# Optimization experiments

Hardware: AMD Instinct MI355X
Metric: run time of the kernel (lower is better)

Reference implementation:

```python
import jax, jax.numpy as jnp
import numpy as np

L = 4      # number of layers (graph nodes)
B = 128    # batch
H = 4096   # neurons per layer


def setup_inputs() -> dict:
    key = jax.random.key(0)
    k1, k2, k3 = jax.random.split(key, 3)
    # per-layer source activations, stacked: [L, B, H]
    states = jax.random.normal(k1, (L, B, H), dtype=jnp.float32)
    # all Connection weight matrices, W[t, s] maps source s -> target t: [L, L, H_out, H_in]
    # scaled by 1/sqrt(H) so summed matmuls stay O(1) (original uses constant w_init)
    W = jax.random.normal(k2, (L, L, H, H), dtype=jnp.float32) * (1.0 / np.sqrt(H))
    # external inputs added into each target's current: [L, B, H]
    ext = jax.random.normal(k3, (L, B, H), dtype=jnp.float32)
    return {"states": states, "W": W, "ext": ext}


def reference(states, W, ext):
    # Synapses/Links: for each target t, sum over sources s of (x_s @ W[t,s].T)
    # (Connection.forward is x @ w.T). Single fused einsum replaces the
    # jit.fork fan-out over L*L small matmuls + Python-level sum.
    currents = jnp.einsum('sbh,tsoh->tbo', states, W) + ext  # [L, B, H]
    # Layer/Neurons: per-node activation function
    return jnp.tanh(currents)
```

## Files before the change

kernel.cpp:

```cpp
#include <hip/hip_runtime.h>
#include <hip/hip_bf16.h>
#include <stdint.h>

#define L_ 4
#define B_ 128
#define H_ 4096
#define BK 64
#define BN 32
#define KSTEPS 256
#define NTHR 256
#define ABYTES (128*BK*2)
#define WBYTES (BN*BK*2)
#define BUFBYTES (ABYTES+WBYTES)

typedef _Float16 f16x8 __attribute__((ext_vector_type(8)));
typedef float    f32x4 __attribute__((ext_vector_type(4)));
typedef float    f4    __attribute__((ext_vector_type(4)));
typedef uint32_t u32x4 __attribute__((ext_vector_type(4)));
typedef uint32_t u32x2 __attribute__((ext_vector_type(2)));

__device__ __forceinline__ uint32_t pack2(float a, float b) {
  const _Float16 ha = (_Float16)a;
  const _Float16 hb = (_Float16)b;
  const uint32_t ua = (uint32_t)__builtin_bit_cast(uint16_t, ha);
  const uint32_t ub = (uint32_t)__builtin_bit_cast(uint16_t, hb);
  return ua | (ub << 16);
}

__global__ void cvt_states_kernel(const float* __restrict__ x,
                                  uint32_t* __restrict__ y, int n4) {
  const int i = blockIdx.x * blockDim.x + threadIdx.x;
  if (i < n4) {
    f4 v = reinterpret_cast<const f4*>(x)[i];
    u32x2 o;
    o.x = pack2(v.x, v.y);
    o.y = pack2(v.z, v.w);
    reinterpret_cast<u32x2*>(y)[i] = o;
  }
}

__device__ __forceinline__ void bar_lgkm0() {
  __builtin_amdgcn_sched_barrier(0);
  asm volatile("s_waitcnt lgkmcnt(0)");
  __builtin_amdgcn_sched_barrier(0);
  __builtin_amdgcn_s_barrier();
  __builtin_amdgcn_sched_barrier(0);
}

template<bool USE_WS>
__global__ __launch_bounds__(NTHR, 2)
void net_gemm_kernel(const float* __restrict__ statesf,
                     const uint16_t* __restrict__ statesh,
                     const float* __restrict__ Wm,
                     const float* __restrict__ ext,
                     float* __restrict__ out)
{
  __shared__ uint8_t lds[2 * BUFBYTES];

  const int tid  = threadIdx.x;
  const int bid  = blockIdx.x;
  const int t    = bid >> 7;
  const int n0   = (bid & 127) * BN;

  const int wv   = tid >> 6;
  const int lane = tid & 63;
  const int lid  = lane & 15;
  const int lh   = lane >> 4;

  const int arow = tid >> 3;
  const int acol = (tid & 7) * 8;
  const uint32_t a_st_off =
      (uint32_t)arow * 128 + (((uint32_t)(tid & 7) * 16) ^ ((uint32_t)(arow & 7) << 4));
  const uint16_t* ah_base = USE_WS ? (statesh + (size_t)arow * H_ + acol) : nullptr;
  const float*    af_base = statesf + (size_t)arow * H_ + acol;

  const int wrow = tid >> 4;
  const int wcol = (tid & 15) * 4;
  const float* w_base = Wm + ((size_t)t * L_ * H_ + (size_t)(n0 + wrow)) * H_ + wcol;
  const uint32_t w_st_off0 =
      (uint32_t)ABYTES + (uint32_t)wrow * 128 + (((uint32_t)(tid & 15) * 8) ^ ((uint32_t)(wrow & 7) << 4));
  const uint32_t w_st_off1 = w_st_off0 + 16 * 128;

  uint32_t a_rd[2][2], b_rd[2][2];
  #pragma unroll
  for (int mf = 0; mf < 2; ++mf)
    #pragma unroll
    for (int kk = 0; kk < 2; ++kk) {
      const int row = wv * 32 + mf * 16 + lid;
      a_rd[mf][kk] = (uint32_t)row * 128 +
                     (((uint32_t)(kk * 64 + lh * 16)) ^ ((uint32_t)(lid & 7) << 4));
    }
  #pragma unroll
  for (int nf = 0; nf < 2; ++nf)
    #pragma unroll
    for (int kk = 0; kk < 2; ++kk) {
      const int row = nf * 16 + lid;
      b_rd[nf][kk] = (uint32_t)ABYTES + (uint32_t)row * 128 +
                     (((uint32_t)(kk * 64 + lh * 16)) ^ ((uint32_t)(lid & 7) << 4));
    }

  f32x4 acc[2][2] = {};

  u32x4 ah0[4], ah1[4];
  f4    af0[4][2], af1[4][2];
  f4    wf0[2], wf1[2];

  auto LOADg = [&](int kidx, u32x4 (&ah)[4], f4 (&af)[4][2], f4 (&wf)[2]) {
    const int s  = kidx >> 6;
    const int h0 = (kidx & 63) << 6;
    if constexpr (USE_WS) {
      const uint16_t* ap = ah_base + (size_t)s * (B_ * H_) + h0;
      #pragma unroll
      for (int j = 0; j < 4; ++j)
        ah[j] = *reinterpret_cast<const u32x4*>(ap + (size_t)j * (32 * H_));
    } else {
      const float* ap = af_base + (size_t)s * (B_ * H_) + h0;
      #pragma unroll
      for (int j = 0; j < 4; ++j) {
        af[j][0] = *reinterpret_cast<const f4*>(ap + (size_t)j * (32 * H_));
        af[j][1] = *reinterpret_cast<const f4*>(ap + (size_t)j * (32 * H_) + 4);
      }
    }
    const float* wp = Wm == nullptr ? nullptr : (w_base + (size_t)s * ((size_t)H_ * H_) + h0);
    wf[0] = __builtin_nontemporal_load(reinterpret_cast<const f4*>(wp));
    wf[1] = __builtin_nontemporal_load(reinterpret_cast<const f4*>(wp + 16 * (size_t)H_));
  };

  auto WRITEg = [&](uint8_t* base, u32x4 (&ah)[4], f4 (&af)[4][2], f4 (&wf)[2]) {
    if constexpr (USE_WS) {
      #pragma unroll
      for (int j = 0; j < 4; ++j)
        *reinterpret_cast<u32x4*>(base + j * 4096 + a_st_off) = ah[j];
    } else {
      #pragma unroll
      for (int j = 0; j < 4; ++j) {
        u32x4 v;
        v.x = pack2(af[j][0].x, af[j][0].y);
        v.y = pack2(af[j][0].z, af[j][0].w);
        v.z = pack2(af[j][1].x, af[j][1].y);
        v.w = pack2(af[j][1].z, af[j][1].w);
        *reinterpret_cast<u32x4*>(base + j * 4096 + a_st_off) = v;
      }
    }
    u32x2 w0, w1;
    w0.x = pack2(wf[0].x, wf[0].y); w0.y = pack2(wf[0].z, wf[0].w);
    w1.x = pack2(wf[1].x, wf[1].y); w1.y = pack2(wf[1].z, wf[1].w);
    *reinterpret_cast<u32x2*>(base + w_st_off0) = w0;
    *reinterpret_cast<u32x2*>(base + w_st_off1) = w1;
  };

  auto COMPUTE = [&](const uint8_t* base) {
    f16x8 av[2][2], bv[2][2];
    #pragma unroll
    for (int mf = 0; mf < 2; ++mf)
      #pragma unroll
      for (int kk = 0; kk < 2; ++kk)
        av[mf][kk] = *reinterpret_cast<const f16x8*>(base + a_rd[mf][kk]);
    #pragma unroll
    for (int nf = 0; nf < 2; ++nf)
      #pragma unroll
      for (int kk = 0; kk < 2; ++kk)
        bv[nf][kk] = *reinterpret_cast<const f16x8*>(base + b_rd[nf][kk]);
    #pragma unroll
    for (int kk = 0; kk < 2; ++kk)
      #pragma unroll
      for (int mf = 0; mf < 2; ++mf)
        #pragma unroll
        for (int nf = 0; nf < 2; ++nf)
          acc[mf][nf] = __builtin_amdgcn_mfma_f32_16x16x32_f16(
              av[mf][kk], bv[nf][kk], acc[mf][nf], 0, 0, 0);
  };

  uint8_t* buf0 = lds;
  uint8_t* buf1 = lds + BUFBYTES;

  LOADg(0, ah0, af0, wf0);
  LOADg(1, ah1, af1, wf1);
  WRITEg(buf0, ah0, af0, wf0);
  bar_lgkm0();

  #pragma unroll 1
  for (int k = 0; k < KSTEPS; k += 2) {
    if (k + 2 < KSTEPS) LOADg(k + 2, ah0, af0, wf0);
    COMPUTE(buf0);
    WRITEg(buf1, ah1, af1, wf1);
    bar_lgkm0();

    if (k + 3 < KSTEPS) LOADg(k + 3, ah1, af1, wf1);
    COMPUTE(buf1);
    if (k + 2 < KSTEPS) {
      WRITEg(buf0, ah0, af0, wf0);
      bar_lgkm0();
    }
  }

  #pragma unroll
  for (int mf = 0; mf < 2; ++mf)
    #pragma unroll
    for (int nf = 0; nf < 2; ++nf)
      #pragma unroll
      for (int j = 0; j < 4; ++j) {
        const int brow = wv * 32 + mf * 16 + lh * 4 + j;
        const int ocol = n0 + nf * 16 + lid;
        const size_t idx = ((size_t)(t * B_ + brow)) * H_ + ocol;
        out[idx] = tanhf(acc[mf][nf][j] + ext[idx]);
      }
}

extern "C" void kernel_launch(void* const* d_in, const int* in_sizes, int n_in,
                              void* d_out, int out_size, void* d_ws, size_t ws_size,
                              hipStream_t stream) {
  const float* states = (const float*)d_in[0];
  const float* W      = (const float*)d_in[1];
  const float* ext    = (const float*)d_in[2];
  float* out          = (float*)d_out;

  const size_t nstates = (size_t)L_ * B_ * H_;
  if (ws_size >= nstates * sizeof(uint16_t)) {
    const int n4 = (int)(nstates / 4);
    cvt_states_kernel<<<(n4 + 255) / 256, 256, 0, stream>>>(states, (uint32_t*)d_ws, n4);
    net_gemm_kernel<true><<<512, NTHR, 0, stream>>>(
        states, (const uint16_t*)d_ws, W, ext, out);
  } else {
    net_gemm_kernel<false><<<512, NTHR, 0, stream>>>(
        states, nullptr, W, ext, out);
  }
}
```

Measured before the change: 250.8 us.

## Load A fragments directly from global into registers and double K tile

Activation (A) fragments are no longer staged through LDS. Each wave now loads its MFMA operands straight from global memory (fp16 workspace or fp32 converted in registers) into registers in the MFMA layout. Only the W tile goes through LDS, and the K tile grows from 64 to 128, which halves the iteration and barrier count. This cuts LDS traffic and footprint, at the cost of more register pressure and less coalesced, strided global reads for A, which mostly come from L2.

```diff
diff --git a/kernel.cpp b/kernel.cpp
--- a/kernel.cpp
+++ b/kernel.cpp
@@ -5,13 +5,11 @@
 #define L_ 4
 #define B_ 128
 #define H_ 4096
-#define BK 64
+#define BK 128
 #define BN 32
-#define KSTEPS 256
+#define KIT 128
 #define NTHR 256
-#define ABYTES (128*BK*2)
 #define WBYTES (BN*BK*2)
-#define BUFBYTES (ABYTES+WBYTES)
 
 typedef _Float16 f16x8 __attribute__((ext_vector_type(8)));
 typedef float    f32x4 __attribute__((ext_vector_type(4)));
@@ -55,7 +53,7 @@
                      const float* __restrict__ ext,
                      float* __restrict__ out)
 {
-  __shared__ uint8_t lds[2 * BUFBYTES];
+  __shared__ uint8_t lds[2 * WBYTES];
 
   const int tid  = threadIdx.x;
   const int bid  = blockIdx.x;
@@ -67,129 +65,115 @@
   const int lid  = lane & 15;
   const int lh   = lane >> 4;
 
-  const int arow = tid >> 3;
-  const int acol = (tid & 7) * 8;
-  const uint32_t a_st_off =
-      (uint32_t)arow * 128 + (((uint32_t)(tid & 7) * 16) ^ ((uint32_t)(arow & 7) << 4));
-  const uint16_t* ah_base = USE_WS ? (statesh + (size_t)arow * H_ + acol) : nullptr;
-  const float*    af_base = statesf + (size_t)arow * H_ + acol;
-
-  const int wrow = tid >> 4;
-  const int wcol = (tid & 15) * 4;
-  const float* w_base = Wm + ((size_t)t * L_ * H_ + (size_t)(n0 + wrow)) * H_ + wcol;
-  const uint32_t w_st_off0 =
-      (uint32_t)ABYTES + (uint32_t)wrow * 128 + (((uint32_t)(tid & 15) * 8) ^ ((uint32_t)(wrow & 7) << 4));
-  const uint32_t w_st_off1 = w_st_off0 + 16 * 128;
-
-  uint32_t a_rd[2][2], b_rd[2][2];
-  #pragma unroll
-  for (int mf = 0; mf < 2; ++mf)
-    #pragma unroll
-    for (int kk = 0; kk < 2; ++kk) {
-      const int row = wv * 32 + mf * 16 + lid;
-      a_rd[mf][kk] = (uint32_t)row * 128 +
-                     (((uint32_t)(kk * 64 + lh * 16)) ^ ((uint32_t)(lid & 7) << 4));
-    }
+  const uint16_t* ah_base = USE_WS ? (statesh + (size_t)(wv * 32 + lid) * H_ + lh * 8) : nullptr;
+  const float*    af_base = statesf + (size_t)(wv * 32 + lid) * H_ + lh * 8;
+
+  const int wrow = tid >> 3;
+  const int wc16 = (tid & 7) * 16;
+  const float* w_base = Wm + ((size_t)(t * L_) * H_ + (size_t)(n0 + wrow)) * H_ + wc16;
+  const uint32_t cb = (uint32_t)(tid & 7) * 32;
+  const uint32_t w_st0 = (uint32_t)wrow * 256 + (cb ^ (((uint32_t)wrow & 7) << 4));
+  const uint32_t w_st1 = (uint32_t)wrow * 256 + ((cb + 16) ^ (((uint32_t)wrow & 7) << 4));
+
+  uint32_t b_rd[2][4];
   #pragma unroll
   for (int nf = 0; nf < 2; ++nf)
     #pragma unroll
-    for (int kk = 0; kk < 2; ++kk) {
-      const int row = nf * 16 + lid;
-      b_rd[nf][kk] = (uint32_t)ABYTES + (uint32_t)row * 128 +
-                     (((uint32_t)(kk * 64 + lh * 16)) ^ ((uint32_t)(lid & 7) << 4));
+    for (int kk = 0; kk < 4; ++kk) {
+      const uint32_t row = (uint32_t)(nf * 16 + lid);
+      b_rd[nf][kk] = row * 256 +
+                     (((uint32_t)(kk * 64 + lh * 16)) ^ (((uint32_t)lid & 7) << 4));
     }
 
   f32x4 acc[2][2] = {};
 
-  u32x4 ah0[4], ah1[4];
-  f4    af0[4][2], af1[4][2];
-  f4    wf0[2], wf1[2];
-
-  auto LOADg = [&](int kidx, u32x4 (&ah)[4], f4 (&af)[4][2], f4 (&wf)[2]) {
-    const int s  = kidx >> 6;
-    const int h0 = (kidx & 63) << 6;
+  f16x8 aA[2][4], aB[2][4];
+  f4    wfA[4], wfB[4];
+
+  auto LOADA = [&](int kidx, f16x8 (&ar)[2][4]) {
+    const int s  = kidx >> 5;
+    const int h0 = (kidx & 31) << 7;
     if constexpr (USE_WS) {
-      const uint16_t* ap = ah_base + (size_t)s * (B_ * H_) + h0;
-      #pragma unroll
-      for (int j = 0; j < 4; ++j)
-        ah[j] = *reinterpret_cast<const u32x4*>(ap + (size_t)j * (32 * H_));
+      const uint16_t* p = ah_base + (size_t)s * (B_ * H_) + h0;
+      #pragma unroll
+      for (int mf = 0; mf < 2; ++mf)
+        #pragma unroll
+        for (int kk = 0; kk < 4; ++kk)
+          ar[mf][kk] = *reinterpret_cast<const f16x8*>(p + mf * (16 * H_) + kk * 32);
     } else {
-      const float* ap = af_base + (size_t)s * (B_ * H_) + h0;
-      #pragma unroll
-      for (int j = 0; j < 4; ++j) {
-        af[j][0] = *reinterpret_cast<const f4*>(ap + (size_t)j * (32 * H_));
-        af[j][1] = *reinterpret_cast<const f4*>(ap + (size_t)j * (32 * H_) + 4);
-      }
+      const float* p = af_base + (size_t)s * (B_ * H_) + h0;
+      #pragma unroll
+      for (int mf = 0; mf < 2; ++mf)
+        #pragma unroll
+        for (int kk = 0; kk < 4; ++kk) {
+          f4 lo = *reinterpret_cast<const f4*>(p + mf * (16 * H_) + kk * 32);
+          f4 hi = *reinterpret_cast<const f4*>(p + mf * (16 * H_) + kk * 32 + 4);
+          u32x4 v;
+          v.x = pack2(lo.x, lo.y); v.y = pack2(lo.z, lo.w);
+          v.z = pack2(hi.x, hi.y); v.w = pack2(hi.z, hi.w);
+          ar[mf][kk] = __builtin_bit_cast(f16x8, v);
+        }
     }
-    const float* wp = Wm == nullptr ? nullptr : (w_base + (size_t)s * ((size_t)H_ * H_) + h0);
-    wf[0] = __builtin_nontemporal_load(reinterpret_cast<const f4*>(wp));
-    wf[1] = __builtin_nontemporal_load(reinterpret_cast<const f4*>(wp + 16 * (size_t)H_));
-  };
-
-  auto WRITEg = [&](uint8_t* base, u32x4 (&ah)[4], f4 (&af)[4][2], f4 (&wf)[2]) {
-    if constexpr (USE_WS) {
-      #pragma unroll
-      for (int j = 0; j < 4; ++j)
-        *reinterpret_cast<u32x4*>(base + j * 4096 + a_st_off) = ah[j];
-    } else {
-      #pragma unroll
-      for (int j = 0; j < 4; ++j) {
-        u32x4 v;
-        v.x = pack2(af[j][0].x, af[j][0].y);
-        v.y = pack2(af[j][0].z, af[j][0].w);
-        v.z = pack2(af[j][1].x, af[j][1].y);
-        v.w = pack2(af[j][1].z, af[j][1].w);
-        *reinterpret_cast<u32x4*>(base + j * 4096 + a_st_off) = v;
-      }
-    }
-    u32x2 w0, w1;
-    w0.x = pack2(wf[0].x, wf[0].y); w0.y = pack2(wf[0].z, wf[0].w);
-    w1.x = pack2(wf[1].x, wf[1].y); w1.y = pack2(wf[1].z, wf[1].w);
-    *reinterpret_cast<u32x2*>(base + w_st_off0) = w0;
-    *reinterpret_cast<u32x2*>(base + w_st_off1) = w1;
-  };
-
-  auto COMPUTE = [&](const uint8_t* base) {
-    f16x8 av[2][2], bv[2][2];
-    #pragma unroll
-    for (int mf = 0; mf < 2; ++mf)
-      #pragma unroll
-      for (int kk = 0; kk < 2; ++kk)
-        av[mf][kk] = *reinterpret_cast<const f16x8*>(base + a_rd[mf][kk]);
+  };
+
+  auto LOADW = [&](int kidx, f4 (&wf)[4]) {
+    const int s  = kidx >> 5;
+    const int h0 = (kidx & 31) << 7;
+    const float* wp = w_base + (size_t)s * ((size_t)H_ * H_) + h0;
+    #pragma unroll
+    for (int j = 0; j < 4; ++j)
+      wf[j] = __builtin_nontemporal_load(reinterpret_cast<const f4*>(wp + j * 4));
+  };
+
+  auto WRITEW = [&](uint8_t* base, f4 (&wf)[4]) {
+    u32x4 v0, v1;
+    v0.x = pack2(wf[0].x, wf[0].y); v0.y = pack2(wf[0].z, wf[0].w);
+    v0.z = pack2(wf[1].x, wf[1].y); v0.w = pack2(wf[1].z, wf[1].w);
+    v1.x = pack2(wf[2].x, wf[2].y); v1.y = pack2(wf[2].z, wf[2].w);
+    v1.z = pack2(wf[3].x, wf[3].y); v1.w = pack2(wf[3].z, wf[3].w);
+    *reinterpret_cast<u32x4*>(base + w_st0) = v0;
+    *reinterpret_cast<u32x4*>(base + w_st1) = v1;
+  };
+
+  auto COMPUTE = [&](const uint8_t* base, f16x8 (&ar)[2][4]) {
+    f16x8 bv[2][4];
     #pragma unroll
     for (int nf = 0; nf < 2; ++nf)
       #pragma unroll
-      for (int kk = 0; kk < 2; ++kk)
+      for (int kk = 0; kk < 4; ++kk)
         bv[nf][kk] = *reinterpret_cast<const f16x8*>(base + b_rd[nf][kk]);
     #pragma unroll
-    for (int kk = 0; kk < 2; ++kk)
+    for (int kk = 0; kk < 4; ++kk)
       #pragma unroll
       for (int mf = 0; mf < 2; ++mf)
         #pragma unroll
         for (int nf = 0; nf < 2; ++nf)
           acc[mf][nf] = __builtin_amdgcn_mfma_f32_16x16x32_f16(
-              av[mf][kk], bv[nf][kk], acc[mf][nf], 0, 0, 0);
+              ar[mf][kk], bv[nf][kk], acc[mf][nf], 0, 0, 0);
   };
 
   uint8_t* buf0 = lds;
-  uint8_t* buf1 = lds + BUFBYTES;
-
-  LOADg(0, ah0, af0, wf0);
-  LOADg(1, ah1, af1, wf1);
-  WRITEg(buf0, ah0, af0, wf0);
+  uint8_t* buf1 = lds + WBYTES;
+
+  LOADW(0, wfA);
+  LOADW(1, wfB);
+  LOADA(0, aA);
+  WRITEW(buf0, wfA);
   bar_lgkm0();
 
   #pragma unroll 1
-  for (int k = 0; k < KSTEPS; k += 2) {
-    if (k + 2 < KSTEPS) LOADg(k + 2, ah0, af0, wf0);
-    COMPUTE(buf0);
-    WRITEg(buf1, ah1, af1, wf1);
+  for (int k = 0; k < KIT; k += 2) {
+    if (k + 2 < KIT) LOADW(k + 2, wfA);
+    LOADA(k + 1, aB);
+    COMPUTE(buf0, aA);
+    WRITEW(buf1, wfB);
     bar_lgkm0();
 
-    if (k + 3 < KSTEPS) LOADg(k + 3, ah1, af1, wf1);
-    COMPUTE(buf1);
-    if (k + 2 < KSTEPS) {
-      WRITEg(buf0, ah0, af0, wf0);
+    if (k + 3 < KIT) LOADW(k + 3, wfB);
+    if (k + 2 < KIT) LOADA(k + 2, aA);
+    COMPUTE(buf1, aB);
+    if (k + 2 < KIT) {
+      WRITEW(buf0, wfA);
       bar_lgkm0();
     }
   }
```

Measured after the change: 430.3 us. 1.72x slower.

## Load activations via direct global-to-LDS copies with triple-buffered pipeline

Applied to the files above, without the earlier changes.

The fp16 activation tile is now copied straight from global memory into LDS with global_load_lds, so it no longer passes through registers. The main loop moves to three LDS buffers, unrolled six ways. Barriers wait on a partial vmcnt so up to two stages of loads can be in flight while MFMAs run. This aims to hide memory latency in the streaming-W GEMM and cut register pressure, at the cost of extra LDS and fragile manual waitcnt bookkeeping; the fp32 fallback path is split into its own kernel.

```diff
diff --git a/kernel.cpp b/kernel.cpp
--- a/kernel.cpp
+++ b/kernel.cpp
@@ -7,11 +7,11 @@
 #define H_ 4096
 #define BK 64
 #define BN 32
-#define KSTEPS 256
+#define KIT 256
 #define NTHR 256
 #define ABYTES (128*BK*2)
 #define WBYTES (BN*BK*2)
-#define BUFBYTES (ABYTES+WBYTES)
+#define BUFB   (ABYTES+WBYTES)
 
 typedef _Float16 f16x8 __attribute__((ext_vector_type(8)));
 typedef float    f32x4 __attribute__((ext_vector_type(4)));
@@ -39,23 +39,27 @@
   }
 }
 
-__device__ __forceinline__ void bar_lgkm0() {
-  __builtin_amdgcn_sched_barrier(0);
-  asm volatile("s_waitcnt lgkmcnt(0)");
-  __builtin_amdgcn_sched_barrier(0);
-  __builtin_amdgcn_s_barrier();
-  __builtin_amdgcn_sched_barrier(0);
-}
-
-template<bool USE_WS>
+__device__ __forceinline__ void gld_lds16(const void* g, void* l) {
+  __builtin_amdgcn_global_load_lds(
+      (const __attribute__((address_space(1))) void*)g,
+      (__attribute__((address_space(3))) void*)l, 16, 0, 0);
+}
+
+#define BAR_VM(N_) do {                                          \
+    __builtin_amdgcn_sched_barrier(0);                           \
+    asm volatile("s_waitcnt vmcnt(" #N_ ") lgkmcnt(0)" ::: "memory"); \
+    __builtin_amdgcn_sched_barrier(0);                           \
+    __builtin_amdgcn_s_barrier();                                \
+    __builtin_amdgcn_sched_barrier(0);                           \
+  } while (0)
+
 __global__ __launch_bounds__(NTHR, 2)
-void net_gemm_kernel(const float* __restrict__ statesf,
-                     const uint16_t* __restrict__ statesh,
+void net_gemm_kernel(const uint16_t* __restrict__ statesh,
                      const float* __restrict__ Wm,
                      const float* __restrict__ ext,
                      float* __restrict__ out)
 {
-  __shared__ uint8_t lds[2 * BUFBYTES];
+  __shared__ __align__(16) uint8_t lds[3 * BUFB];
 
   const int tid  = threadIdx.x;
   const int bid  = blockIdx.x;
@@ -67,19 +71,20 @@
   const int lid  = lane & 15;
   const int lh   = lane >> 4;
 
-  const int arow = tid >> 3;
-  const int acol = (tid & 7) * 8;
-  const uint32_t a_st_off =
-      (uint32_t)arow * 128 + (((uint32_t)(tid & 7) * 16) ^ ((uint32_t)(arow & 7) << 4));
-  const uint16_t* ah_base = USE_WS ? (statesh + (size_t)arow * H_ + acol) : nullptr;
-  const float*    af_base = statesf + (size_t)arow * H_ + acol;
+  uint32_t a_src[4];
+  #pragma unroll
+  for (int j = 0; j < 4; ++j) {
+    const uint32_t row = (uint32_t)(j * 32 + wv * 8 + (lane >> 3));
+    const uint32_t cb  = (uint32_t)(lane & 7) * 16;
+    a_src[j] = row * (H_ * 2) + (cb ^ ((row & 7) << 4));
+  }
 
   const int wrow = tid >> 4;
   const int wcol = (tid & 15) * 4;
   const float* w_base = Wm + ((size_t)t * L_ * H_ + (size_t)(n0 + wrow)) * H_ + wcol;
-  const uint32_t w_st_off0 =
+  const uint32_t w_st0 =
       (uint32_t)ABYTES + (uint32_t)wrow * 128 + (((uint32_t)(tid & 15) * 8) ^ ((uint32_t)(wrow & 7) << 4));
-  const uint32_t w_st_off1 = w_st_off0 + 16 * 128;
+  const uint32_t w_st1 = w_st0 + 16 * 128;
 
   uint32_t a_rd[2][2], b_rd[2][2];
   #pragma unroll
@@ -100,56 +105,38 @@
     }
 
   f32x4 acc[2][2] = {};
-
-  u32x4 ah0[4], ah1[4];
-  f4    af0[4][2], af1[4][2];
-  f4    wf0[2], wf1[2];
-
-  auto LOADg = [&](int kidx, u32x4 (&ah)[4], f4 (&af)[4][2], f4 (&wf)[2]) {
+  f4 wf[2][4];
+
+  auto LOADW = [&](int kidx, f4 (&w)[4]) {
     const int s  = kidx >> 6;
     const int h0 = (kidx & 63) << 6;
-    if constexpr (USE_WS) {
-      const uint16_t* ap = ah_base + (size_t)s * (B_ * H_) + h0;
-      #pragma unroll
-      for (int j = 0; j < 4; ++j)
-        ah[j] = *reinterpret_cast<const u32x4*>(ap + (size_t)j * (32 * H_));
-    } else {
-      const float* ap = af_base + (size_t)s * (B_ * H_) + h0;
-      #pragma unroll
-      for (int j = 0; j < 4; ++j) {
-        af[j][0] = *reinterpret_cast<const f4*>(ap + (size_t)j * (32 * H_));
-        af[j][1] = *reinterpret_cast<const f4*>(ap + (size_t)j * (32 * H_) + 4);
-      }
-    }
-    const float* wp = Wm == nullptr ? nullptr : (w_base + (size_t)s * ((size_t)H_ * H_) + h0);
-    wf[0] = __builtin_nontemporal_load(reinterpret_cast<const f4*>(wp));
-    wf[1] = __builtin_nontemporal_load(reinterpret_cast<const f4*>(wp + 16 * (size_t)H_));
-  };
-
-  auto WRITEg = [&](uint8_t* base, u32x4 (&ah)[4], f4 (&af)[4][2], f4 (&wf)[2]) {
-    if constexpr (USE_WS) {
-      #pragma unroll
-      for (int j = 0; j < 4; ++j)
-        *reinterpret_cast<u32x4*>(base + j * 4096 + a_st_off) = ah[j];
-    } else {
-      #pragma unroll
-      for (int j = 0; j < 4; ++j) {
-        u32x4 v;
-        v.x = pack2(af[j][0].x, af[j][0].y);
-        v.y = pack2(af[j][0].z, af[j][0].w);
-        v.z = pack2(af[j][1].x, af[j][1].y);
-        v.w = pack2(af[j][1].z, af[j][1].w);
-        *reinterpret_cast<u32x4*>(base + j * 4096 + a_st_off) = v;
-      }
-    }
+    const float* wp = w_base + (size_t)s * ((size_t)H_ * H_) + h0;
+    w[0] = __builtin_nontemporal_load(reinterpret_cast<const f4*>(wp));
+    w[1] = __builtin_nontemporal_load(reinterpret_cast<const f4*>(wp + 16 * (size_t)H_));
+    w[2] = w[0];
+    w[3] = w[1];
+  };
+
+  auto ALDS = [&](int kidx, int bufi) {
+    const uint8_t* g = (const uint8_t*)statesh +
+                       (size_t)(kidx >> 6) * (B_ * H_ * 2) + (size_t)(kidx & 63) * 128;
+    uint8_t* l = lds + bufi * BUFB + wv * 1024;
+    #pragma unroll
+    for (int j = 0; j < 4; ++j)
+      gld_lds16(g + a_src[j], l + j * 4096);
+  };
+
+  auto WRITEW = [&](int bufi, f4 (&w)[4]) {
+    uint8_t* base = lds + bufi * BUFB;
     u32x2 w0, w1;
-    w0.x = pack2(wf[0].x, wf[0].y); w0.y = pack2(wf[0].z, wf[0].w);
-    w1.x = pack2(wf[1].x, wf[1].y); w1.y = pack2(wf[1].z, wf[1].w);
-    *reinterpret_cast<u32x2*>(base + w_st_off0) = w0;
-    *reinterpret_cast<u32x2*>(base + w_st_off1) = w1;
-  };
-
-  auto COMPUTE = [&](const uint8_t* base) {
+    w0.x = pack2(w[0].x, w[0].y); w0.y = pack2(w[0].z, w[0].w);
+    w1.x = pack2(w[1].x, w[1].y); w1.y = pack2(w[1].z, w[1].w);
+    *reinterpret_cast<u32x2*>(base + w_st0) = w0;
+    *reinterpret_cast<u32x2*>(base + w_st1) = w1;
+  };
+
+  auto COMPUTE = [&](int bufi) {
+    const uint8_t* base = lds + bufi * BUFB;
     f16x8 av[2][2], bv[2][2];
     #pragma unroll
     for (int mf = 0; mf < 2; ++mf)
@@ -171,26 +158,174 @@
               av[mf][kk], bv[nf][kk], acc[mf][nf], 0, 0, 0);
   };
 
+  LOADW(0, wf[0]);
+  LOADW(1, wf[1]);
+  ALDS(0, 0);
+  ALDS(1, 1);
+  WRITEW(0, wf[0]);
+  BAR_VM(4);
+
+  #define BODY(kk_, C_, N_, WT_, LE_) do {      \
+      LOADW((kk_) + 2, wf[LE_]);                \
+      ALDS((kk_) + 2, (N_));                    \
+      COMPUTE((C_));                            \
+      WRITEW((WT_), wf[1 - (LE_)]);             \
+      BAR_VM(6);                                \
+    } while (0)
+
+  #pragma unroll 1
+  for (int k = 0; k < 252; k += 6) {
+    BODY(k + 0, 0, 2, 1, 0);
+    BODY(k + 1, 1, 0, 2, 1);
+    BODY(k + 2, 2, 1, 0, 0);
+    BODY(k + 3, 0, 2, 1, 1);
+    BODY(k + 4, 1, 0, 2, 0);
+    BODY(k + 5, 2, 1, 0, 1);
+  }
+  BODY(252, 0, 2, 1, 0);
+  BODY(253, 1, 0, 2, 1);
+  COMPUTE(2);
+  WRITEW(0, wf[1]);
+  BAR_VM(0);
+  COMPUTE(0);
+  #undef BODY
+
+  #pragma unroll
+  for (int mf = 0; mf < 2; ++mf)
+    #pragma unroll
+    for (int nf = 0; nf < 2; ++nf)
+      #pragma unroll
+      for (int j = 0; j < 4; ++j) {
+        const int brow = wv * 32 + mf * 16 + lh * 4 + j;
+        const int ocol = n0 + nf * 16 + lid;
+        const size_t idx = ((size_t)(t * B_ + brow)) * H_ + ocol;
+        out[idx] = tanhf(acc[mf][nf][j] + ext[idx]);
+      }
+}
+
+__global__ __launch_bounds__(NTHR, 2)
+void net_gemm_fb(const float* __restrict__ statesf,
+                 const float* __restrict__ Wm,
+                 const float* __restrict__ ext,
+                 float* __restrict__ out)
+{
+  __shared__ __align__(16) uint8_t lds[2 * BUFB];
+
+  const int tid  = threadIdx.x;
+  const int bid  = blockIdx.x;
+  const int t    = bid >> 7;
+  const int n0   = (bid & 127) * BN;
+  const int wv   = tid >> 6;
+  const int lane = tid & 63;
+  const int lid  = lane & 15;
+  const int lh   = lane >> 4;
+
+  const int arow = tid >> 3;
+  const int acol = (tid & 7) * 8;
+  const uint32_t a_st_off =
+      (uint32_t)arow * 128 + (((uint32_t)(tid & 7) * 16) ^ ((uint32_t)(arow & 7) << 4));
+  const float* af_base = statesf + (size_t)arow * H_ + acol;
+
+  const int wrow = tid >> 4;
+  const int wcol = (tid & 15) * 4;
+  const float* w_base = Wm + ((size_t)t * L_ * H_ + (size_t)(n0 + wrow)) * H_ + wcol;
+  const uint32_t w_st0 =
+      (uint32_t)ABYTES + (uint32_t)wrow * 128 + (((uint32_t)(tid & 15) * 8) ^ ((uint32_t)(wrow & 7) << 4));
+  const uint32_t w_st1 = w_st0 + 16 * 128;
+
+  uint32_t a_rd[2][2], b_rd[2][2];
+  #pragma unroll
+  for (int mf = 0; mf < 2; ++mf)
+    #pragma unroll
+    for (int kk = 0; kk < 2; ++kk) {
+      const int row = wv * 32 + mf * 16 + lid;
+      a_rd[mf][kk] = (uint32_t)row * 128 +
+                     (((uint32_t)(kk * 64 + lh * 16)) ^ ((uint32_t)(lid & 7) << 4));
+    }
+  #pragma unroll
+  for (int nf = 0; nf < 2; ++nf)
+    #pragma unroll
+    for (int kk = 0; kk < 2; ++kk) {
+      const int row = nf * 16 + lid;
+      b_rd[nf][kk] = (uint32_t)ABYTES + (uint32_t)row * 128 +
+                     (((uint32_t)(kk * 64 + lh * 16)) ^ ((uint32_t)(lid & 7) << 4));
+    }
+
+  f32x4 acc[2][2] = {};
+  f4 af0[4][2], af1[4][2], wf0[2], wf1[2];
+
+  auto LOADg = [&](int kidx, f4 (&af)[4][2], f4 (&wfx)[2]) {
+    const int s  = kidx >> 6;
+    const int h0 = (kidx & 63) << 6;
+    const float* ap = af_base + (size_t)s * (B_ * H_) + h0;
+    #pragma unroll
+    for (int j = 0; j < 4; ++j) {
+      af[j][0] = *reinterpret_cast<const f4*>(ap + (size_t)j * (32 * H_));
+      af[j][1] = *reinterpret_cast<const f4*>(ap + (size_t)j * (32 * H_) + 4);
+    }
+    const float* wp = w_base + (size_t)s * ((size_t)H_ * H_) + h0;
+    wfx[0] = __builtin_nontemporal_load(reinterpret_cast<const f4*>(wp));
+    wfx[1] = __builtin_nontemporal_load(reinterpret_cast<const f4*>(wp + 16 * (size_t)H_));
+  };
+
+  auto WRITEg = [&](uint8_t* base, f4 (&af)[4][2], f4 (&wfx)[2]) {
+    #pragma unroll
+    for (int j = 0; j < 4; ++j) {
+      u32x4 v;
+      v.x = pack2(af[j][0].x, af[j][0].y);
+      v.y = pack2(af[j][0].z, af[j][0].w);
+      v.z = pack2(af[j][1].x, af[j][1].y);
+      v.w = pack2(af[j][1].z, af[j][1].w);
+      *reinterpret_cast<u32x4*>(base + j * 4096 + a_st_off) = v;
+    }
+    u32x2 w0, w1;
+    w0.x = pack2(wfx[0].x, wfx[0].y); w0.y = pack2(wfx[0].z, wfx[0].w);
+    w1.x = pack2(wfx[1].x, wfx[1].y); w1.y = pack2(wfx[1].z, wfx[1].w);
+    *reinterpret_cast<u32x2*>(base + w_st0) = w0;
+    *reinterpret_cast<u32x2*>(base + w_st1) = w1;
+  };
+
+  auto COMPUTE = [&](const uint8_t* base) {
+    f16x8 av[2][2], bv[2][2];
+    #pragma unroll
+    for (int mf = 0; mf < 2; ++mf)
+      #pragma unroll
+      for (int kk = 0; kk < 2; ++kk)
+        av[mf][kk] = *reinterpret_cast<const f16x8*>(base + a_rd[mf][kk]);
+    #pragma unroll
+    for (int nf = 0; nf < 2; ++nf)
+      #pragma unroll
+      for (int kk = 0; kk < 2; ++kk)
+        bv[nf][kk] = *reinterpret_cast<const f16x8*>(base + b_rd[nf][kk]);
+    #pragma unroll
+    for (int kk = 0; kk < 2; ++kk)
+      #pragma unroll
+      for (int mf = 0; mf < 2; ++mf)
+        #pragma unroll
+        for (int nf = 0; nf < 2; ++nf)
+          acc[mf][nf] = __builtin_amdgcn_mfma_f32_16x16x32_f16(
+              av[mf][kk], bv[nf][kk], acc[mf][nf], 0, 0, 0);
+  };
+
   uint8_t* buf0 = lds;
-  uint8_t* buf1 = lds + BUFBYTES;
-
-  LOADg(0, ah0, af0, wf0);
-  LOADg(1, ah1, af1, wf1);
-  WRITEg(buf0, ah0, af0, wf0);
-  bar_lgkm0();
+  uint8_t* buf1 = lds + BUFB;
+
+  LOADg(0, af0, wf0);
+  LOADg(1, af1, wf1);
+  WRITEg(buf0, af0, wf0);
+  BAR_VM(0);
 
   #pragma unroll 1
-  for (int k = 0; k < KSTEPS; k += 2) {
-    if (k + 2 < KSTEPS) LOADg(k + 2, ah0, af0, wf0);
+  for (int k = 0; k < KIT; k += 2) {
+    if (k + 2 < KIT) LOADg(k + 2, af0, wf0);
     COMPUTE(buf0);
-    WRITEg(buf1, ah1, af1, wf1);
-    bar_lgkm0();
-
-    if (k + 3 < KSTEPS) LOADg(k + 3, ah1, af1, wf1);
+    WRITEg(buf1, af1, wf1);
+    BAR_VM(0);
+    if (k + 3 < KIT) LOADg(k + 3, af1, wf1);
     COMPUTE(buf1);
-    if (k + 2 < KSTEPS) {
-      WRITEg(buf0, ah0, af0, wf0);
-      bar_lgkm0();
+    if (k + 2 < KIT) {
+      WRITEg(buf0, af0, wf0);
+      BAR_VM(0);
     }
   }
 
@@ -219,10 +354,8 @@
   if (ws_size >= nstates * sizeof(uint16_t)) {
     const int n4 = (int)(nstates / 4);
     cvt_states_kernel<<<(n4 + 255) / 256, 256, 0, stream>>>(states, (uint32_t*)d_ws, n4);
-    net_gemm_kernel<true><<<512, NTHR, 0, stream>>>(
-        states, (const uint16_t*)d_ws, W, ext, out);
+    net_gemm_kernel<<<512, NTHR, 0, stream>>>((const uint16_t*)d_ws, W, ext, out);
   } else {
-    net_gemm_kernel<false><<<512, NTHR, 0, stream>>>(
-        states, nullptr, W, ext, out);
-  }
-}
+    net_gemm_fb<<<512, NTHR, 0, stream>>>(states, W, ext, out);
+  }
+}
```

Result: slower. 265.2 us (+5.8%).
